# Kernel tuning notes

Measured on AMD Instinct MI355X. Metric: run time of the kernel, lower is better.

Reference implementation:

```python
import jax, jax.numpy as jnp
import numpy as np

N_NODES = 100000
N_EDGES = 640000
D_IN = 128
D_OUT = 128


def setup_inputs() -> dict:
    key = jax.random.key(0)
    k1, k2, k3, k4, k5, k6 = jax.random.split(key, 6)
    x = jax.random.normal(k1, (N_NODES, D_IN), dtype=jnp.float32)
    edge_weights = jax.random.uniform(k2, (N_EDGES, 1), dtype=jnp.float32)
    src = jax.random.randint(k3, (N_EDGES,), 0, N_NODES)
    dst = jax.random.randint(k4, (N_EDGES,), 0, N_NODES)
    # nn.Linear init scale ~ 1/sqrt(in_feats)
    W = jax.random.normal(k5, (D_OUT, D_IN), dtype=jnp.float32) / np.sqrt(D_IN)
    b = jax.random.normal(k6, (D_OUT,), dtype=jnp.float32) / np.sqrt(D_IN)
    return {"x": x, "edge_weights": edge_weights, "src": src, "dst": dst, "W": W, "b": b}


def reference(x, edge_weights, src, dst, W, b):
    # message: gather source node features, scale by per-edge weight  [E, D]
    m = x[src] * edge_weights
    # reduce: sum messages into destination nodes  [N, D]
    h = jax.ops.segment_sum(m, dst, num_segments=N_NODES)
    # dense linear  [N, D_OUT]
    return h @ W.T + b
```

## Files before the change

kernel.cpp:

```cpp
#include <hip/hip_runtime.h>
#include <hip/hip_bf16.h>

#define D 128
#define SCAN_CH 4096

typedef __bf16 bf16x8 __attribute__((ext_vector_type(8)));
typedef float  f32x4  __attribute__((ext_vector_type(4)));
typedef float  f32x2  __attribute__((ext_vector_type(2)));

__device__ __forceinline__ __bf16 f2bf(float f) { return (__bf16)f; }
__device__ __forceinline__ int pad8(int v) { return (v + 7) & ~7; }

__global__ __launch_bounds__(256) void prep_kernel(
    const float* __restrict__ W, __bf16* __restrict__ wb,
    int* __restrict__ cnt, int M, int4* __restrict__ bins4, long nbin4)
{
    long t    = (long)blockIdx.x * 256 + threadIdx.x;
    long nthr = (long)gridDim.x * 256;

    for (long i = t; i < nbin4; i += nthr) bins4[i] = make_int4(0, 0, 0, 0);
    for (long i = t; i < M; i += nthr) cnt[i] = 0;

    if (t < 2048) {
        int lane = (int)t & 63;
        int frag = (int)t >> 6;
        int kb = frag >> 3, fn = frag & 7;
        int n  = fn * 16 + (lane & 15);
        int k0 = kb * 32 + (lane >> 4) * 8;
        const float* src = &W[(size_t)n * D + k0];
        float4 v0 = *reinterpret_cast<const float4*>(src);
        float4 v1 = *reinterpret_cast<const float4*>(src + 4);
        bf16x8 o;
        o[0]=f2bf(v0.x); o[1]=f2bf(v0.y); o[2]=f2bf(v0.z); o[3]=f2bf(v0.w);
        o[4]=f2bf(v1.x); o[5]=f2bf(v1.y); o[6]=f2bf(v1.z); o[7]=f2bf(v1.w);
        *reinterpret_cast<bf16x8*>(&wb[((size_t)frag * 64 + lane) * 8]) = o;
    }
}

__global__ __launch_bounds__(256) void gemm_mfma_kernel(
    const float* __restrict__ x, const __bf16* __restrict__ wb,
    __bf16* __restrict__ y, int M)
{
    const int tid  = threadIdx.x;
    const int lane = tid & 63;
    const int wv   = tid >> 6;
    const int l15  = lane & 15;
    const int l4   = lane >> 4;
    const int row_base = blockIdx.x * 128 + wv * 32;

    f32x4 acc[2][8];
    #pragma unroll
    for (int mi = 0; mi < 2; ++mi)
        #pragma unroll
        for (int fn = 0; fn < 8; ++fn)
            #pragma unroll
            for (int c = 0; c < 4; ++c) acc[mi][fn][c] = 0.f;

    #pragma unroll
    for (int kb = 0; kb < 4; ++kb) {
        bf16x8 b[8];
        #pragma unroll
        for (int fn = 0; fn < 8; ++fn)
            b[fn] = *reinterpret_cast<const bf16x8*>(
                        &wb[((size_t)(kb * 8 + fn) * 64 + lane) * 8]);
        #pragma unroll
        for (int mi = 0; mi < 2; ++mi) {
            int row = row_base + mi * 16 + l15;
            int rc  = row < M ? row : M - 1;
            const f32x4* ap = reinterpret_cast<const f32x4*>(
                                   &x[(size_t)rc * D + kb * 32 + l4 * 8]);
            f32x4 v0 = __builtin_nontemporal_load(ap);
            f32x4 v1 = __builtin_nontemporal_load(ap + 1);
            bf16x8 a;
            a[0]=f2bf(v0[0]); a[1]=f2bf(v0[1]); a[2]=f2bf(v0[2]); a[3]=f2bf(v0[3]);
            a[4]=f2bf(v1[0]); a[5]=f2bf(v1[1]); a[6]=f2bf(v1[2]); a[7]=f2bf(v1[3]);
            #pragma unroll
            for (int fn = 0; fn < 8; ++fn)
                acc[mi][fn] = __builtin_amdgcn_mfma_f32_16x16x32_bf16(
                                  a, b[fn], acc[mi][fn], 0, 0, 0);
        }
    }

    #pragma unroll
    for (int mi = 0; mi < 2; ++mi)
        #pragma unroll
        for (int r = 0; r < 4; ++r) {
            int row = row_base + mi * 16 + l4 * 4 + r;
            if (row >= M) continue;
            #pragma unroll
            for (int fn = 0; fn < 8; ++fn)
                y[(size_t)row * D + fn * 16 + l15] = f2bf(acc[mi][fn][r]);
        }
}

__global__ __launch_bounds__(256) void hist_kernel(
    const int* __restrict__ dst, int* __restrict__ cnt,
    int* __restrict__ rank, int E)
{
    int e = blockIdx.x * 256 + threadIdx.x;
    if (e < E) {
        int d = __builtin_nontemporal_load(&dst[e]);
        rank[e] = atomicAdd(&cnt[d], 1);
    }
}

__global__ __launch_bounds__(256) void scan_part_kernel(
    const int* __restrict__ cnt, int* __restrict__ bsum, int N)
{
    __shared__ int wred[4];
    const int tid  = threadIdx.x;
    const int lane = tid & 63;
    const int wid  = tid >> 6;
    int off = blockIdx.x * SCAN_CH + tid * 16;
    int s = 0;
    #pragma unroll
    for (int i = 0; i < 16; ++i) {
        int idx = off + i;
        if (idx < N) s += pad8(cnt[idx]);
    }
    #pragma unroll
    for (int d = 32; d >= 1; d >>= 1) s += __shfl_xor(s, d, 64);
    if (lane == 0) wred[wid] = s;
    __syncthreads();
    if (tid == 0) bsum[blockIdx.x] = wred[0] + wred[1] + wred[2] + wred[3];
}

__global__ __launch_bounds__(256) void scan_write_kernel(
    const int* __restrict__ cnt, const int* __restrict__ bsum,
    int* __restrict__ base, int N, int NB)
{
    __shared__ int boff_s;
    __shared__ int wsum[4];
    const int b    = blockIdx.x;
    const int tid  = threadIdx.x;
    const int lane = tid & 63;
    const int wid  = tid >> 6;

    if (wid == 0) {
        int v = (lane < b) ? bsum[lane] : 0;
        #pragma unroll
        for (int d = 32; d >= 1; d >>= 1) v += __shfl_xor(v, d, 64);
        if (lane == 0) boff_s = v;
    }
    __syncthreads();

    int off = b * SCAN_CH + tid * 16;
    int v[16];
    int s = 0;
    #pragma unroll
    for (int i = 0; i < 16; ++i) {
        int idx = off + i;
        v[i] = (idx < N) ? pad8(cnt[idx]) : 0;
        s += v[i];
    }
    int ssum = s;
    #pragma unroll
    for (int d = 1; d < 64; d <<= 1) {
        int t = __shfl_up(ssum, d, 64);
        if (lane >= d) ssum += t;
    }
    if (lane == 63) wsum[wid] = ssum;
    __syncthreads();
    int woff = 0;
    for (int w = 0; w < wid; ++w) woff += wsum[w];

    int run = boff_s + woff + ssum - s;
    #pragma unroll
    for (int i = 0; i < 16; ++i) {
        int idx = off + i;
        if (idx < N) base[idx] = run;
        if (idx == N - 1) base[N] = run + v[i];
        run += v[i];
    }
}

__global__ __launch_bounds__(256) void bin_kernel(
    const int* __restrict__ src, const int* __restrict__ dst,
    const float* __restrict__ ew, const int* __restrict__ base,
    const int* __restrict__ rank, int2* __restrict__ bins, int E)
{
    int e = blockIdx.x * 256 + threadIdx.x;
    if (e >= E) return;
    int d  = __builtin_nontemporal_load(&dst[e]);
    int sv = __builtin_nontemporal_load(&src[e]);
    float w = __builtin_nontemporal_load(&ew[e]);
    int rk = __builtin_nontemporal_load(&rank[e]);
    int p = base[d] + rk;
    bins[p] = make_int2(sv * (D / 2), __float_as_int(w));
}

__global__ __launch_bounds__(256) void gather_kernel(
    const __bf16* __restrict__ y, const int* __restrict__ base,
    const int2* __restrict__ bins, const float* __restrict__ bias,
    float* __restrict__ out, int N)
{
    int gw   = (blockIdx.x * 256 + threadIdx.x) >> 6;
    int lane = threadIdx.x & 63;
    if (gw >= N) return;

    const unsigned* yb = reinterpret_cast<const unsigned*>(y);
    const int b0 = __builtin_amdgcn_readfirstlane(base[gw]);
    const int b1 = __builtin_amdgcn_readfirstlane(base[gw + 1]);
    float accx = 0.f, accy = 0.f;

    for (int i = b0; i < b1; i += 8) {
        int2 e[8];
        #pragma unroll
        for (int t = 0; t < 8; ++t) e[t] = bins[i + t];
        unsigned p[8];
        #pragma unroll
        for (int t = 0; t < 8; ++t)
            p[t] = yb[(unsigned)e[t].x + lane];
        #pragma unroll
        for (int t = 0; t < 8; ++t) {
            float w = __int_as_float(e[t].y);
            accx += __uint_as_float(p[t] << 16) * w;
            accy += __uint_as_float(p[t] & 0xFFFF0000u) * w;
        }
    }

    float2 bv = *reinterpret_cast<const float2*>(&bias[lane * 2]);
    f32x2 o;
    o[0] = accx + bv.x;
    o[1] = accy + bv.y;
    __builtin_nontemporal_store(o, reinterpret_cast<f32x2*>(&out[(size_t)gw * D + lane * 2]));
}

extern "C" void kernel_launch(void* const* d_in, const int* in_sizes, int n_in,
                              void* d_out, int out_size, void* d_ws, size_t ws_size,
                              hipStream_t stream) {
    const float* x   = (const float*)d_in[0];
    const float* ew  = (const float*)d_in[1];
    const int*   src = (const int*)d_in[2];
    const int*   dst = (const int*)d_in[3];
    const float* W   = (const float*)d_in[4];
    const float* b   = (const float*)d_in[5];
    float*       out = (float*)d_out;

    const int E  = in_sizes[2];
    const int M  = out_size / D;
    const int NB = (M + SCAN_CH - 1) / SCAN_CH;
    const size_t BIN_CAP = ((size_t)E + 7 * (size_t)M + 8) & ~(size_t)1;

    char* p = (char*)d_ws;
    __bf16* y    = (__bf16*)p;             p += (size_t)M * D * 2;
    __bf16* wb   = (__bf16*)p;             p += (size_t)32 * 64 * 8 * 2;
    int2*   bins = (int2*)p;               p += BIN_CAP * 8;
    int*    base = (int*)p;                p += (size_t)(M + 1) * 4;
    int*    cnt  = (int*)p;                p += (size_t)M * 4;
    int*    rank = (int*)p;                p += (size_t)E * 4;
    int*    bsum = (int*)p;

    prep_kernel<<<512, 256, 0, stream>>>(W, wb, cnt, M,
                                         (int4*)bins, (long)(BIN_CAP / 2));

    gemm_mfma_kernel<<<(M + 127) / 128, 256, 0, stream>>>(x, wb, y, M);

    hist_kernel<<<(E + 255) / 256, 256, 0, stream>>>(dst, cnt, rank, E);
    scan_part_kernel<<<NB, 256, 0, stream>>>(cnt, bsum, M);
    scan_write_kernel<<<NB, 256, 0, stream>>>(cnt, bsum, base, M, NB);
    bin_kernel<<<(E + 255) / 256, 256, 0, stream>>>(src, dst, ew, base, rank, bins, E);

    gather_kernel<<<(M * 64 + 255) / 256, 256, 0, stream>>>(y, base, bins, b, out, M);
}
```

Before: 127.0 us.

## Fuse degree histogram into GEMM kernel and convert W to bf16 inline

Merges the dst histogram (atomic counts and ranks) into the GEMM kernel through a grid-stride loop, so the atomic traffic overlaps with the MFMA work and one launch goes away. W is now read as fp32 and converted to bf16 inside each GEMM wave instead of being pre-packed by the prep kernel. The zeroing kernel gets a larger grid. This removes launch overhead but adds redundant W loads and conversions per block, and the atomics may slow the GEMM.

```diff
diff --git a/kernel.cpp b/kernel.cpp
--- a/kernel.cpp
+++ b/kernel.cpp
@@ -11,42 +11,38 @@
 __device__ __forceinline__ __bf16 f2bf(float f) { return (__bf16)f; }
 __device__ __forceinline__ int pad8(int v) { return (v + 7) & ~7; }
 
-__global__ __launch_bounds__(256) void prep_kernel(
-    const float* __restrict__ W, __bf16* __restrict__ wb,
+__global__ __launch_bounds__(256) void zero_kernel(
     int* __restrict__ cnt, int M, int4* __restrict__ bins4, long nbin4)
 {
     long t    = (long)blockIdx.x * 256 + threadIdx.x;
     long nthr = (long)gridDim.x * 256;
-
     for (long i = t; i < nbin4; i += nthr) bins4[i] = make_int4(0, 0, 0, 0);
     for (long i = t; i < M; i += nthr) cnt[i] = 0;
-
-    if (t < 2048) {
-        int lane = (int)t & 63;
-        int frag = (int)t >> 6;
-        int kb = frag >> 3, fn = frag & 7;
-        int n  = fn * 16 + (lane & 15);
-        int k0 = kb * 32 + (lane >> 4) * 8;
-        const float* src = &W[(size_t)n * D + k0];
-        float4 v0 = *reinterpret_cast<const float4*>(src);
-        float4 v1 = *reinterpret_cast<const float4*>(src + 4);
-        bf16x8 o;
-        o[0]=f2bf(v0.x); o[1]=f2bf(v0.y); o[2]=f2bf(v0.z); o[3]=f2bf(v0.w);
-        o[4]=f2bf(v1.x); o[5]=f2bf(v1.y); o[6]=f2bf(v1.z); o[7]=f2bf(v1.w);
-        *reinterpret_cast<bf16x8*>(&wb[((size_t)frag * 64 + lane) * 8]) = o;
-    }
-}
-
-__global__ __launch_bounds__(256) void gemm_mfma_kernel(
-    const float* __restrict__ x, const __bf16* __restrict__ wb,
-    __bf16* __restrict__ y, int M)
+}
+
+__global__ __launch_bounds__(256) void gemm_hist_kernel(
+    const float* __restrict__ x, const float* __restrict__ W,
+    __bf16* __restrict__ y, int M,
+    const int* __restrict__ dst, int* __restrict__ cnt,
+    int* __restrict__ rank, int E)
 {
     const int tid  = threadIdx.x;
+
+    {
+        int t    = blockIdx.x * 256 + tid;
+        int nthr = gridDim.x * 256;
+        for (int e = t; e < E; e += nthr) {
+            int d = __builtin_nontemporal_load(&dst[e]);
+            rank[e] = atomicAdd(&cnt[d], 1);
+        }
+    }
+
     const int lane = tid & 63;
     const int wv   = tid >> 6;
     const int l15  = lane & 15;
     const int l4   = lane >> 4;
     const int row_base = blockIdx.x * 128 + wv * 32;
+    if (row_base >= M) return;
 
     f32x4 acc[2][8];
     #pragma unroll
@@ -60,9 +56,13 @@
     for (int kb = 0; kb < 4; ++kb) {
         bf16x8 b[8];
         #pragma unroll
-        for (int fn = 0; fn < 8; ++fn)
-            b[fn] = *reinterpret_cast<const bf16x8*>(
-                        &wb[((size_t)(kb * 8 + fn) * 64 + lane) * 8]);
+        for (int fn = 0; fn < 8; ++fn) {
+            const float* wp = &W[(size_t)(fn * 16 + l15) * D + kb * 32 + l4 * 8];
+            float4 w0 = *reinterpret_cast<const float4*>(wp);
+            float4 w1 = *reinterpret_cast<const float4*>(wp + 4);
+            b[fn][0]=f2bf(w0.x); b[fn][1]=f2bf(w0.y); b[fn][2]=f2bf(w0.z); b[fn][3]=f2bf(w0.w);
+            b[fn][4]=f2bf(w1.x); b[fn][5]=f2bf(w1.y); b[fn][6]=f2bf(w1.z); b[fn][7]=f2bf(w1.w);
+        }
         #pragma unroll
         for (int mi = 0; mi < 2; ++mi) {
             int row = row_base + mi * 16 + l15;
@@ -93,17 +93,6 @@
         }
 }
 
-__global__ __launch_bounds__(256) void hist_kernel(
-    const int* __restrict__ dst, int* __restrict__ cnt,
-    int* __restrict__ rank, int E)
-{
-    int e = blockIdx.x * 256 + threadIdx.x;
-    if (e < E) {
-        int d = __builtin_nontemporal_load(&dst[e]);
-        rank[e] = atomicAdd(&cnt[d], 1);
-    }
-}
-
 __global__ __launch_bounds__(256) void scan_part_kernel(
     const int* __restrict__ cnt, int* __restrict__ bsum, int N)
 {
@@ -244,21 +233,20 @@
 
     char* p = (char*)d_ws;
     __bf16* y    = (__bf16*)p;             p += (size_t)M * D * 2;
-    __bf16* wb   = (__bf16*)p;             p += (size_t)32 * 64 * 8 * 2;
     int2*   bins = (int2*)p;               p += BIN_CAP * 8;
     int*    base = (int*)p;                p += (size_t)(M + 1) * 4;
     int*    cnt  = (int*)p;                p += (size_t)M * 4;
     int*    rank = (int*)p;                p += (size_t)E * 4;
     int*    bsum = (int*)p;
 
-    prep_kernel<<<512, 256, 0, stream>>>(W, wb, cnt, M,
-                                         (int4*)bins, (long)(BIN_CAP / 2));
-
-    gemm_mfma_kernel<<<(M + 127) / 128, 256, 0, stream>>>(x, wb, y, M);
-
-    hist_kernel<<<(E + 255) / 256, 256, 0, stream>>>(dst, cnt, rank, E);
+    zero_kernel<<<2048, 256, 0, stream>>>(cnt, M, (int4*)bins, (long)(BIN_CAP / 2));
+
+    gemm_hist_kernel<<<(M + 127) / 128, 256, 0, stream>>>(
+        x, W, y, M, dst, cnt, rank, E);
+
     scan_part_kernel<<<NB, 256, 0, stream>>>(cnt, bsum, M);
     scan_write_kernel<<<NB, 256, 0, stream>>>(cnt, bsum, base, M, NB);
+
     bin_kernel<<<(E + 255) / 256, 256, 0, stream>>>(src, dst, ew, base, rank, bins, E);
 
     gather_kernel<<<(M * 64 + 255) / 256, 256, 0, stream>>>(y, base, bins, b, out, M);
```

After: 144.6 us. +13.8%, slower.
